# Kernel optimization log

Hardware: AMD Instinct MI355X
Metric: run time of the kernel (lower is better)

## Reference

```python
import jax, jax.numpy as jnp
import numpy as np

B, T, C = 4, 4096, 512
DFF = 4 * C


def setup_inputs() -> dict:
    key = jax.random.key(0)
    ks = jax.random.split(key, 8)
    s = 1.0 / np.sqrt(C)
    sf = 1.0 / np.sqrt(DFF)
    return {
        "inputs": jax.random.normal(ks[0], (B, T, C), dtype=jnp.float32),
        "Wq": jax.random.uniform(ks[1], (C, C), jnp.float32, -s, s),
        "Wk": jax.random.uniform(ks[2], (C, C), jnp.float32, -s, s),
        "Wv": jax.random.uniform(ks[3], (C, C), jnp.float32, -s, s),
        "W1": jax.random.uniform(ks[4], (C, DFF), jnp.float32, -s, s),
        "b1": jax.random.uniform(ks[5], (DFF,), jnp.float32, -s, s),
        "W2": jax.random.uniform(ks[6], (DFF, C), jnp.float32, -sf, sf),
        "b2": jax.random.uniform(ks[7], (C,), jnp.float32, -sf, sf),
    }


def reference(inputs, Wq, Wk, Wv, W1, b1, W2, b2):
    # Single-head causal self-attention, NO 1/sqrt(d) scaling (faithful to source)
    q = inputs @ Wq  # [B,T,C]
    k = inputs @ Wk
    v = inputs @ Wv
    scores = jnp.einsum("btc,bsc->bts", q, k)  # [B,T,T]
    Tdim = inputs.shape[1]
    causal = jnp.tril(jnp.ones((Tdim, Tdim), dtype=bool))
    scores = jnp.where(causal, scores, -jnp.inf)
    attn = jax.nn.softmax(scores, axis=-1)
    new_v = jnp.einsum("bts,bsc->btc", attn, v)  # [B,T,C]
    h = jax.nn.relu(new_v @ W1 + b1)  # [B,T,4C]
    return h @ W2 + b2  # [B,T,C]
```

## Files before the change

### kernel.cpp

```cpp
#include <hip/hip_runtime.h>
#include <stdint.h>

typedef __attribute__((ext_vector_type(8))) short bf16x8;
typedef __attribute__((ext_vector_type(8))) _Float16 f16x8;
typedef __attribute__((ext_vector_type(4))) float f32x4;
typedef __attribute__((ext_vector_type(4))) unsigned short us4;
typedef unsigned short u16;

#define DEVI static __device__ __forceinline__

#define Bb 4
#define Tt 4096
#define Cch 512
#define DFFd 2048
#define Mrows (Bb*Tt)
#define TRI 8650752ull

DEVI u16 f2bf(float f){
  union{float f;unsigned u;} v; v.f = f;
  unsigned r = v.u + 0x7FFFu + ((v.u >> 16) & 1u);
  return (u16)(r >> 16);
}
DEVI u16 f2h(float f){
  union{_Float16 h; u16 u;} v; v.h = (_Float16)f; return v.u;
}
DEVI float h2f(u16 h){
  union{u16 u; _Float16 h;} v; v.u = h; return (float)v.h;
}
DEVI size_t PANE(int q){ return (size_t)8192 * (size_t)(q*(q+1)); }

DEVI void gload16(const void* g, void* l){
  __builtin_amdgcn_global_load_lds((const __attribute__((address_space(1))) unsigned int*)g,
                                   (__attribute__((address_space(3))) unsigned int*)l, 16, 0, 0);
}

#define RDSWZ(l15, l4) (((l4)*16) ^ ((((l15) >> 1) & 3) << 4))

DEVI void stage128x64(const u16* __restrict__ base, int ld, char* lds, int w, int lane){
  #pragma unroll
  for(int i = 0; i < 4; i++){
    int s = i & 1;
    int chunk = w*2 + (i >> 1);
    int row = chunk*16 + (lane >> 2);
    int col = s*32 + (((lane & 3)*8) ^ (((lane >> 3) & 3) << 3));
    gload16(base + (size_t)row * ld + col, lds + s*8192 + chunk*1024 + lane*16);
  }
}
DEVI void stage64x64(const u16* __restrict__ base, int ld, char* lds, int w, int lane){
  #pragma unroll
  for(int i = 0; i < 2; i++){
    int s = i;
    int row = w*16 + (lane >> 2);
    int col = s*32 + (((lane & 3)*8) ^ (((lane >> 3) & 3) << 3));
    gload16(base + (size_t)row * ld + col, lds + s*4096 + w*1024 + lane*16);
  }
}

__global__ void k_cast_f16(const float* __restrict__ in, u16* __restrict__ out, int n){
  int i = (blockIdx.x * blockDim.x + threadIdx.x) * 4;
  if(i < n){
    float4 f = *(const float4*)(in + i);
    us4 o; o.x = f2h(f.x); o.y = f2h(f.y); o.z = f2h(f.z); o.w = f2h(f.w);
    *(us4*)(out + i) = o;
  }
}

__global__ void k_transpose_f32_f16(const float* __restrict__ in, u16* __restrict__ out,
                                    int inStride, int outStride){
  __shared__ float tile[32][33];
  int c0 = blockIdx.x * 32, r0 = blockIdx.y * 32;
  int tx = threadIdx.x, ty = threadIdx.y;
  #pragma unroll
  for(int j = 0; j < 4; j++)
    tile[ty + 8*j][tx] = in[(size_t)(r0 + ty + 8*j) * inStride + c0 + tx];
  __syncthreads();
  #pragma unroll
  for(int j = 0; j < 4; j++)
    out[(size_t)(c0 + ty + 8*j) * outStride + r0 + tx] = f2h(tile[tx][ty + 8*j]);
}

__global__ void k_transpose_f32_bf16(const float* __restrict__ in, u16* __restrict__ out,
                                     int inStride, int outStride){
  __shared__ float tile[32][33];
  int c0 = blockIdx.x * 32, r0 = blockIdx.y * 32;
  int tx = threadIdx.x, ty = threadIdx.y;
  #pragma unroll
  for(int j = 0; j < 4; j++)
    tile[ty + 8*j][tx] = in[(size_t)(r0 + ty + 8*j) * inStride + c0 + tx];
  __syncthreads();
  #pragma unroll
  for(int j = 0; j < 4; j++)
    out[(size_t)(c0 + ty + 8*j) * outStride + r0 + tx] = f2bf(tile[tx][ty + 8*j]);
}

DEVI void core_f16_64(const u16* __restrict__ A, const u16* __restrict__ B,
                      int lda, int ldb, int K, u16* As, u16* Bs, f32x4 (&acc)[4][4]){
  const int t = threadIdx.x;
  const int lane = t & 63, w = t >> 6;
  const int l15 = lane & 15, l4 = lane >> 4;
  const int wr = (w >> 1) * 64, wc = (w & 1) * 64;
  const int ro = RDSWZ(l15, l4);
  for(int kt = 0; kt < K; kt += 64){
    __syncthreads();
    stage128x64(A + kt, lda, (char*)As, w, lane);
    stage128x64(B + kt, ldb, (char*)Bs, w, lane);
    __syncthreads();
    f16x8 af[2][4], bfr[2][4];
    #pragma unroll
    for(int s = 0; s < 2; s++){
      #pragma unroll
      for(int mi = 0; mi < 4; mi++)
        af[s][mi] = *(const f16x8*)((const char*)As + s*8192 + (wr + mi*16 + l15)*64 + ro);
      #pragma unroll
      for(int ni = 0; ni < 4; ni++)
        bfr[s][ni] = *(const f16x8*)((const char*)Bs + s*8192 + (wc + ni*16 + l15)*64 + ro);
    }
    #pragma unroll
    for(int s = 0; s < 2; s++)
      #pragma unroll
      for(int mi = 0; mi < 4; mi++)
        #pragma unroll
        for(int ni = 0; ni < 4; ni++)
          acc[mi][ni] = __builtin_amdgcn_mfma_f32_16x16x32_f16(af[s][mi], bfr[s][ni], acc[mi][ni], 0, 0, 0);
  }
}

DEVI void core_bf16_64(const u16* __restrict__ A, const u16* __restrict__ B,
                       int lda, int ldb, int K, u16* As, u16* Bs, f32x4 (&acc)[4][4]){
  const int t = threadIdx.x;
  const int lane = t & 63, w = t >> 6;
  const int l15 = lane & 15, l4 = lane >> 4;
  const int wr = (w >> 1) * 64, wc = (w & 1) * 64;
  const int ro = RDSWZ(l15, l4);
  for(int kt = 0; kt < K; kt += 64){
    __syncthreads();
    stage128x64(A + kt, lda, (char*)As, w, lane);
    stage128x64(B + kt, ldb, (char*)Bs, w, lane);
    __syncthreads();
    bf16x8 af[2][4], bfr[2][4];
    #pragma unroll
    for(int s = 0; s < 2; s++){
      #pragma unroll
      for(int mi = 0; mi < 4; mi++)
        af[s][mi] = *(const bf16x8*)((const char*)As + s*8192 + (wr + mi*16 + l15)*64 + ro);
      #pragma unroll
      for(int ni = 0; ni < 4; ni++)
        bfr[s][ni] = *(const bf16x8*)((const char*)Bs + s*8192 + (wc + ni*16 + l15)*64 + ro);
    }
    #pragma unroll
    for(int s = 0; s < 2; s++)
      #pragma unroll
      for(int mi = 0; mi < 4; mi++)
        #pragma unroll
        for(int ni = 0; ni < 4; ni++)
          acc[mi][ni] = __builtin_amdgcn_mfma_f32_16x16x32_bf16(af[s][mi], bfr[s][ni], acc[mi][ni], 0, 0, 0);
  }
}

__global__ __launch_bounds__(256) void k_qkv(const u16* __restrict__ Xf,
                                             const u16* __restrict__ Wt,
                                             u16* __restrict__ QK,
                                             u16* __restrict__ Vg){
  __shared__ u16 As[8192], Bs[8192];
  const int bm = blockIdx.x * 128, bn = blockIdx.y * 128;
  f32x4 acc[4][4] = {};
  core_f16_64(Xf + (size_t)bm*512, Wt + (size_t)bn*512, 512, 512, 512, As, Bs, acc);
  const int t = threadIdx.x, lane = t & 63, w = t >> 6;
  const int l15 = lane & 15, l4 = lane >> 4;
  const int wr = (w >> 1) * 64, wc = (w & 1) * 64;
  #pragma unroll
  for(int mi = 0; mi < 4; mi++)
    #pragma unroll
    for(int ni = 0; ni < 4; ni++){
      int col = bn + wc + ni*16 + l15;
      #pragma unroll
      for(int r = 0; r < 4; r++){
        int row = bm + wr + mi*16 + l4*4 + r;
        u16 h = f2h(acc[mi][ni][r]);
        if(col < 1024){
          QK[(size_t)row * 1024 + col] = h;
        } else {
          int c = col - 1024;
          int b = row >> 12, tq = row & 4095;
          Vg[(size_t)b*Cch*Tt + ((size_t)(tq >> 5) * 512 + c) * 32 + (tq & 31)] = h;
        }
      }
    }
}

__global__ __launch_bounds__(256) void k_score(const u16* __restrict__ QK, int b0,
                                               u16* __restrict__ Sp){
  const int kt = blockIdx.x, qt = 31 - blockIdx.y;
  if(kt > qt) return;
  const int zb = blockIdx.z;
  const u16* QKb = QK + (size_t)(b0 + zb) * Tt * 1024;
  u16* Spz = Sp + (size_t)zb * TRI;
  __shared__ u16 As[8192], Bs[8192];
  const u16* A = QKb + (size_t)(qt*128) * 1024;
  const u16* B = QKb + (size_t)(kt*128) * 1024 + 512;
  f32x4 acc[4][4] = {};
  core_f16_64(A, B, 1024, 1024, 512, As, Bs, acc);
  const int t = threadIdx.x, lane = t & 63, w = t >> 6;
  const int l15 = lane & 15, l4 = lane >> 4;
  const int wr = (w >> 1) * 64, wc = (w & 1) * 64;
  const int ldc = (qt + 1) * 128;
  u16* C = Spz + PANE(qt) + (size_t)kt*128;
  const bool diag = (kt == qt);
  #pragma unroll
  for(int mi = 0; mi < 4; mi++)
    #pragma unroll
    for(int ni = 0; ni < 4; ni++){
      int cl = wc + ni*16 + l15;
      #pragma unroll
      for(int r = 0; r < 4; r++){
        int rl = wr + mi*16 + l4*4 + r;
        float v = acc[mi][ni][r];
        if(diag && cl > rl) v = -__builtin_inff();
        C[(size_t)rl * ldc + cl] = f2h(v);
      }
    }
}

__global__ __launch_bounds__(256) void k_softmax(u16* __restrict__ Sp){
  u16* Spz = Sp + (size_t)blockIdx.z * TRI;
  const int w = threadIdx.x >> 6, lane = threadIdx.x & 63;
  const int r = (1023 - blockIdx.x) * 4 + w;
  const int qt = r >> 7;
  const int nc = qt + 1;
  const int L = nc * 128;
  const size_t base = PANE(qt) + (size_t)(r & 127) * L;
  ushort2* rp = (ushort2*)(Spz + base);
  float2 v[32];
  float mx = -__builtin_inff();
  #pragma unroll
  for(int c = 0; c < 32; c++) if(c < nc){
    ushort2 h = rp[c*64 + lane];
    v[c].x = h2f(h.x); v[c].y = h2f(h.y);
    mx = fmaxf(mx, fmaxf(v[c].x, v[c].y));
  }
  #pragma unroll
  for(int s = 1; s < 64; s <<= 1) mx = fmaxf(mx, __shfl_xor(mx, s));
  float sm = 0.f;
  #pragma unroll
  for(int c = 0; c < 32; c++) if(c < nc){
    v[c].x = __expf(v[c].x - mx);
    v[c].y = __expf(v[c].y - mx);
    sm += v[c].x + v[c].y;
  }
  #pragma unroll
  for(int s = 1; s < 64; s <<= 1) sm += __shfl_xor(sm, s);
  const float inv = 1.f / sm;
  #pragma unroll
  for(int c = 0; c < 32; c++) if(c < nc){
    ushort2 o; o.x = f2h(v[c].x * inv); o.y = f2h(v[c].y * inv);
    rp[c*64 + lane] = o;
  }
}

__global__ __launch_bounds__(256) void k_pv(const u16* __restrict__ Pp, const u16* __restrict__ Vg,
                                            u16* __restrict__ NV, int b0){
  const int nc = blockIdx.x, qt = 31 - blockIdx.y, zb = blockIdx.z;
  const int L = (qt + 1) * 128;
  __shared__ u16 As[8192], Bs[8192];
  const u16* A = Pp + (size_t)zb * TRI + PANE(qt);
  const u16* Vgb = Vg + (size_t)(b0 + zb) * Cch * Tt;
  const int t = threadIdx.x, lane = t & 63, w = t >> 6;
  const int l15 = lane & 15, l4 = lane >> 4;
  const int wr = (w >> 1) * 64, wc = (w & 1) * 64;
  const int ro = RDSWZ(l15, l4);
  f32x4 acc[4][4] = {};
  for(int kt = 0; kt < L; kt += 64){
    __syncthreads();
    stage128x64(A + kt, L, (char*)As, w, lane);
    const size_t kvb0 = (size_t)(kt >> 5) * 16384 + nc*4096;
    #pragma unroll
    for(int i = 0; i < 4; i++){
      int s = i & 1;
      int p = w*2 + (i >> 1);
      int crow = p*16 + (lane >> 2);
      int kvo = ((lane & 3)*8) ^ (((lane >> 3) & 3) << 3);
      gload16(Vgb + kvb0 + (size_t)s*16384 + (size_t)crow*32 + kvo,
              (char*)Bs + s*8192 + p*1024 + lane*16);
    }
    __syncthreads();
    f16x8 af[2][4], bfr[2][4];
    #pragma unroll
    for(int s = 0; s < 2; s++){
      #pragma unroll
      for(int mi = 0; mi < 4; mi++)
        af[s][mi] = *(const f16x8*)((const char*)As + s*8192 + (wr + mi*16 + l15)*64 + ro);
      #pragma unroll
      for(int ni = 0; ni < 4; ni++)
        bfr[s][ni] = *(const f16x8*)((const char*)Bs + s*8192 + (wc + ni*16 + l15)*64 + ro);
    }
    #pragma unroll
    for(int s = 0; s < 2; s++)
      #pragma unroll
      for(int mi = 0; mi < 4; mi++)
        #pragma unroll
        for(int ni = 0; ni < 4; ni++)
          acc[mi][ni] = __builtin_amdgcn_mfma_f32_16x16x32_f16(af[s][mi], bfr[s][ni], acc[mi][ni], 0, 0, 0);
  }
  u16* Cb = NV + ((size_t)(b0 + zb) * Tt + qt*128) * Cch + nc*128;
  #pragma unroll
  for(int mi = 0; mi < 4; mi++)
    #pragma unroll
    for(int ni = 0; ni < 4; ni++){
      int cl = wc + ni*16 + l15;
      #pragma unroll
      for(int r = 0; r < 4; r++){
        int rl = wr + mi*16 + l4*4 + r;
        Cb[(size_t)rl * Cch + cl] = f2bf(acc[mi][ni][r]);
      }
    }
}

__global__ __launch_bounds__(256) void k_ffn1(const u16* __restrict__ A,
                                              const u16* __restrict__ Bt,
                                              u16* __restrict__ Hout,
                                              const float* __restrict__ bias){
  __shared__ u16 As[8192], Bs[8192];
  const int bm = blockIdx.x * 128, bn = blockIdx.y * 128;
  f32x4 acc[4][4] = {};
  core_bf16_64(A + (size_t)bm*512, Bt + (size_t)bn*512, 512, 512, 512, As, Bs, acc);
  const int t = threadIdx.x, lane = t & 63, w = t >> 6;
  const int l15 = lane & 15, l4 = lane >> 4;
  const int wr = (w >> 1) * 64, wc = (w & 1) * 64;
  #pragma unroll
  for(int mi = 0; mi < 4; mi++)
    #pragma unroll
    for(int ni = 0; ni < 4; ni++){
      int col = bn + wc + ni*16 + l15;
      float bv = bias[col];
      #pragma unroll
      for(int r = 0; r < 4; r++){
        int row = bm + wr + mi*16 + l4*4 + r;
        float v = acc[mi][ni][r] + bv;
        v = v > 0.f ? v : 0.f;
        Hout[(size_t)row * DFFd + col] = f2bf(v);
      }
    }
}

__global__ __launch_bounds__(256) void k_ffn2(const u16* __restrict__ A,
                                              const u16* __restrict__ Bt,
                                              float* __restrict__ out,
                                              const float* __restrict__ bias){
  __shared__ u16 As[8192], Bs[4096];
  const int bm = blockIdx.x * 128, bn = blockIdx.y * 64;
  const int t = threadIdx.x, lane = t & 63, w = t >> 6;
  const int l15 = lane & 15, l4 = lane >> 4;
  const int wr = (w >> 1) * 64, wc = (w & 1) * 32;
  const int ro = RDSWZ(l15, l4);
  const u16* Ap = A + (size_t)bm*2048;
  const u16* Bp = Bt + (size_t)bn*2048;
  f32x4 acc[4][2] = {};
  for(int kt = 0; kt < 2048; kt += 64){
    __syncthreads();
    stage128x64(Ap + kt, 2048, (char*)As, w, lane);
    stage64x64(Bp + kt, 2048, (char*)Bs, w, lane);
    __syncthreads();
    bf16x8 af[2][4], bfr[2][2];
    #pragma unroll
    for(int s = 0; s < 2; s++){
      #pragma unroll
      for(int mi = 0; mi < 4; mi++)
        af[s][mi] = *(const bf16x8*)((const char*)As + s*8192 + (wr + mi*16 + l15)*64 + ro);
      #pragma unroll
      for(int ni = 0; ni < 2; ni++)
        bfr[s][ni] = *(const bf16x8*)((const char*)Bs + s*4096 + (wc + ni*16 + l15)*64 + ro);
    }
    #pragma unroll
    for(int s = 0; s < 2; s++)
      #pragma unroll
      for(int mi = 0; mi < 4; mi++)
        #pragma unroll
        for(int ni = 0; ni < 2; ni++)
          acc[mi][ni] = __builtin_amdgcn_mfma_f32_16x16x32_bf16(af[s][mi], bfr[s][ni], acc[mi][ni], 0, 0, 0);
  }
  #pragma unroll
  for(int mi = 0; mi < 4; mi++)
    #pragma unroll
    for(int ni = 0; ni < 2; ni++){
      int col = bn + wc + ni*16 + l15;
      float bv = bias[col];
      #pragma unroll
      for(int r = 0; r < 4; r++){
        int row = bm + wr + mi*16 + l4*4 + r;
        out[(size_t)row * Cch + col] = acc[mi][ni][r] + bv;
      }
    }
}

extern "C" void kernel_launch(void* const* d_in, const int* in_sizes, int n_in,
                              void* d_out, int out_size, void* d_ws, size_t ws_size,
                              hipStream_t stream){
  (void)in_sizes; (void)n_in; (void)out_size;
  const float* X  = (const float*)d_in[0];
  const float* Wq = (const float*)d_in[1];
  const float* Wk = (const float*)d_in[2];
  const float* Wv = (const float*)d_in[3];
  const float* W1 = (const float*)d_in[4];
  const float* b1 = (const float*)d_in[5];
  const float* W2 = (const float*)d_in[6];
  const float* b2 = (const float*)d_in[7];
  float* out = (float*)d_out;

  const size_t MB = 1024ull*1024ull;
  const size_t PANE_B = (size_t)TRI * 2;
  char* ws = (char*)d_ws;

  int nb = 1;
  if(ws_size >= 4*PANE_B + 71*MB) nb = 4;
  else if(ws_size >= 2*PANE_B + 71*MB) nb = 2;

  u16*   Sp = (u16*)ws;
  u16*   Xf = (u16*)ws;
  u16*   H  = (u16*)ws;
  size_t off = (size_t)nb * PANE_B;
  u16*   QK   = (u16*)(ws + off);  off += 32*MB;
  u16*   Vg   = (u16*)(ws + off);  off += 16*MB;
  u16*   NV   = (u16*)(ws + off);  off += 16*MB;
  u16*   Wt   = (u16*)(ws + off);  off += 2*MB;
  u16*   W1t  = (u16*)(ws + off);  off += 2*MB;
  u16*   W2t  = (u16*)(ws + off);

  dim3 tb(32, 8);

  k_cast_f16<<<Mrows*Cch/4/256, 256, 0, stream>>>(X, Xf, Mrows*Cch);

  k_transpose_f32_f16<<<dim3(16,16), tb, 0, stream>>>(Wq, Wt,            512, 512);
  k_transpose_f32_f16<<<dim3(16,16), tb, 0, stream>>>(Wk, Wt +  512*512, 512, 512);
  k_transpose_f32_f16<<<dim3(16,16), tb, 0, stream>>>(Wv, Wt + 1024*512, 512, 512);
  k_transpose_f32_bf16<<<dim3(64,16), tb, 0, stream>>>(W1, W1t, 2048, 512);
  k_transpose_f32_bf16<<<dim3(16,64), tb, 0, stream>>>(W2, W2t, 512, 2048);

  k_qkv<<<dim3(128, 12), 256, 0, stream>>>(Xf, Wt, QK, Vg);

  for(int b0 = 0; b0 < Bb; b0 += nb){
    k_score<<<dim3(32, 32, nb), 256, 0, stream>>>(QK, b0, Sp);
    k_softmax<<<dim3(1024, 1, nb), 256, 0, stream>>>(Sp);
    k_pv<<<dim3(4, 32, nb), 256, 0, stream>>>(Sp, Vg, NV, b0);
  }

  k_ffn1<<<dim3(128, 16), 256, 0, stream>>>(NV, W1t, H, b1);
  k_ffn2<<<dim3(128, 8), 256, 0, stream>>>(H, W2t, out, b2);
}
```

Measured before the change: 342.0 us.

## Enlarge GEMM tiles to 256x128 with 8 waves for qkv, score, ffn1

Switches the qkv, score and ffn1 GEMM kernels from 128x128 tiles with 4 waves to 256x128 tiles with 8 waves. The B tile in LDS is shared across twice as many output rows, which halves B global traffic per output and the number of blocks. The score kernel adapts the causal triangle indexing so each half of the block writes its own 128-row pane and skips rows above the diagonal. The cost is more LDS per block, a larger block that may reduce occupancy, and idle waves on partially masked diagonal tiles.

```diff
diff --git a/kernel.cpp b/kernel.cpp
--- a/kernel.cpp
+++ b/kernel.cpp
@@ -35,6 +35,7 @@
 }
 
 #define RDSWZ(l15, l4) (((l4)*16) ^ ((((l15) >> 1) & 3) << 4))
+#define SRCSWZ(lane) ((((lane) & 3)*8) ^ ((((lane) >> 3) & 3) << 3))
 
 DEVI void stage128x64(const u16* __restrict__ base, int ld, char* lds, int w, int lane){
   #pragma unroll
@@ -42,7 +43,7 @@
     int s = i & 1;
     int chunk = w*2 + (i >> 1);
     int row = chunk*16 + (lane >> 2);
-    int col = s*32 + (((lane & 3)*8) ^ (((lane >> 3) & 3) << 3));
+    int col = s*32 + SRCSWZ(lane);
     gload16(base + (size_t)row * ld + col, lds + s*8192 + chunk*1024 + lane*16);
   }
 }
@@ -51,8 +52,28 @@
   for(int i = 0; i < 2; i++){
     int s = i;
     int row = w*16 + (lane >> 2);
-    int col = s*32 + (((lane & 3)*8) ^ (((lane >> 3) & 3) << 3));
+    int col = s*32 + SRCSWZ(lane);
     gload16(base + (size_t)row * ld + col, lds + s*4096 + w*1024 + lane*16);
+  }
+}
+
+DEVI void stage256x64_w8(const u16* __restrict__ base, int ld, char* lds, int w, int lane){
+  #pragma unroll
+  for(int i = 0; i < 4; i++){
+    int s = i & 1;
+    int chunk = w + (i >> 1)*8;
+    int row = chunk*16 + (lane >> 2);
+    int col = s*32 + SRCSWZ(lane);
+    gload16(base + (size_t)row * ld + col, lds + s*16384 + chunk*1024 + lane*16);
+  }
+}
+DEVI void stage128x64_w8(const u16* __restrict__ base, int ld, char* lds, int w, int lane){
+  #pragma unroll
+  for(int i = 0; i < 2; i++){
+    int s = i;
+    int row = w*16 + (lane >> 2);
+    int col = s*32 + SRCSWZ(lane);
+    gload16(base + (size_t)row * ld + col, lds + s*8192 + w*1024 + lane*16);
   }
 }
 
@@ -93,8 +114,8 @@
     out[(size_t)(c0 + ty + 8*j) * outStride + r0 + tx] = f2bf(tile[tx][ty + 8*j]);
 }
 
-DEVI void core_f16_64(const u16* __restrict__ A, const u16* __restrict__ B,
-                      int lda, int ldb, int K, u16* As, u16* Bs, f32x4 (&acc)[4][4]){
+DEVI void core_f16_256(const u16* __restrict__ A, const u16* __restrict__ B,
+                       int lda, int ldb, int K, u16* As, u16* Bs, f32x4 (&acc)[4][4]){
   const int t = threadIdx.x;
   const int lane = t & 63, w = t >> 6;
   const int l15 = lane & 15, l4 = lane >> 4;
@@ -102,15 +123,15 @@
   const int ro = RDSWZ(l15, l4);
   for(int kt = 0; kt < K; kt += 64){
     __syncthreads();
-    stage128x64(A + kt, lda, (char*)As, w, lane);
-    stage128x64(B + kt, ldb, (char*)Bs, w, lane);
+    stage256x64_w8(A + kt, lda, (char*)As, w, lane);
+    stage128x64_w8(B + kt, ldb, (char*)Bs, w, lane);
     __syncthreads();
     f16x8 af[2][4], bfr[2][4];
     #pragma unroll
     for(int s = 0; s < 2; s++){
       #pragma unroll
       for(int mi = 0; mi < 4; mi++)
-        af[s][mi] = *(const f16x8*)((const char*)As + s*8192 + (wr + mi*16 + l15)*64 + ro);
+        af[s][mi] = *(const f16x8*)((const char*)As + s*16384 + (wr + mi*16 + l15)*64 + ro);
       #pragma unroll
       for(int ni = 0; ni < 4; ni++)
         bfr[s][ni] = *(const f16x8*)((const char*)Bs + s*8192 + (wc + ni*16 + l15)*64 + ro);
@@ -125,8 +146,8 @@
   }
 }
 
-DEVI void core_bf16_64(const u16* __restrict__ A, const u16* __restrict__ B,
-                       int lda, int ldb, int K, u16* As, u16* Bs, f32x4 (&acc)[4][4]){
+DEVI void core_bf16_256(const u16* __restrict__ A, const u16* __restrict__ B,
+                        int lda, int ldb, int K, u16* As, u16* Bs, f32x4 (&acc)[4][4]){
   const int t = threadIdx.x;
   const int lane = t & 63, w = t >> 6;
   const int l15 = lane & 15, l4 = lane >> 4;
@@ -134,15 +155,15 @@
   const int ro = RDSWZ(l15, l4);
   for(int kt = 0; kt < K; kt += 64){
     __syncthreads();
-    stage128x64(A + kt, lda, (char*)As, w, lane);
-    stage128x64(B + kt, ldb, (char*)Bs, w, lane);
+    stage256x64_w8(A + kt, lda, (char*)As, w, lane);
+    stage128x64_w8(B + kt, ldb, (char*)Bs, w, lane);
     __syncthreads();
     bf16x8 af[2][4], bfr[2][4];
     #pragma unroll
     for(int s = 0; s < 2; s++){
       #pragma unroll
       for(int mi = 0; mi < 4; mi++)
-        af[s][mi] = *(const bf16x8*)((const char*)As + s*8192 + (wr + mi*16 + l15)*64 + ro);
+        af[s][mi] = *(const bf16x8*)((const char*)As + s*16384 + (wr + mi*16 + l15)*64 + ro);
       #pragma unroll
       for(int ni = 0; ni < 4; ni++)
         bfr[s][ni] = *(const bf16x8*)((const char*)Bs + s*8192 + (wc + ni*16 + l15)*64 + ro);
@@ -157,14 +178,14 @@
   }
 }
 
-__global__ __launch_bounds__(256) void k_qkv(const u16* __restrict__ Xf,
+__global__ __launch_bounds__(512) void k_qkv(const u16* __restrict__ Xf,
                                              const u16* __restrict__ Wt,
                                              u16* __restrict__ QK,
                                              u16* __restrict__ Vg){
-  __shared__ u16 As[8192], Bs[8192];
-  const int bm = blockIdx.x * 128, bn = blockIdx.y * 128;
+  __shared__ u16 As[16384], Bs[8192];
+  const int bm = blockIdx.x * 256, bn = blockIdx.y * 128;
   f32x4 acc[4][4] = {};
-  core_f16_64(Xf + (size_t)bm*512, Wt + (size_t)bn*512, 512, 512, 512, As, Bs, acc);
+  core_f16_256(Xf + (size_t)bm*512, Wt + (size_t)bn*512, 512, 512, 512, As, Bs, acc);
   const int t = threadIdx.x, lane = t & 63, w = t >> 6;
   const int l15 = lane & 15, l4 = lane >> 4;
   const int wr = (w >> 1) * 64, wc = (w & 1) * 64;
@@ -188,24 +209,27 @@
     }
 }
 
-__global__ __launch_bounds__(256) void k_score(const u16* __restrict__ QK, int b0,
+__global__ __launch_bounds__(512) void k_score(const u16* __restrict__ QK, int b0,
                                                u16* __restrict__ Sp){
-  const int kt = blockIdx.x, qt = 31 - blockIdx.y;
-  if(kt > qt) return;
+  const int kt = blockIdx.x, qy = 15 - blockIdx.y;
+  if(kt > 2*qy + 1) return;
   const int zb = blockIdx.z;
   const u16* QKb = QK + (size_t)(b0 + zb) * Tt * 1024;
   u16* Spz = Sp + (size_t)zb * TRI;
-  __shared__ u16 As[8192], Bs[8192];
-  const u16* A = QKb + (size_t)(qt*128) * 1024;
+  __shared__ u16 As[16384], Bs[8192];
+  const u16* A = QKb + (size_t)(qy*256) * 1024;
   const u16* B = QKb + (size_t)(kt*128) * 1024 + 512;
   f32x4 acc[4][4] = {};
-  core_f16_64(A, B, 1024, 1024, 512, As, Bs, acc);
+  core_f16_256(A, B, 1024, 1024, 512, As, Bs, acc);
   const int t = threadIdx.x, lane = t & 63, w = t >> 6;
   const int l15 = lane & 15, l4 = lane >> 4;
   const int wr = (w >> 1) * 64, wc = (w & 1) * 64;
-  const int ldc = (qt + 1) * 128;
-  u16* C = Spz + PANE(qt) + (size_t)kt*128;
-  const bool diag = (kt == qt);
+  const int qt_row = qy*2 + (wr >> 7);
+  if(kt > qt_row) return;
+  const int ldc = (qt_row + 1) * 128;
+  const int rof = wr & 64;
+  u16* C = Spz + PANE(qt_row) + (size_t)kt*128;
+  const bool diag = (kt == qt_row);
   #pragma unroll
   for(int mi = 0; mi < 4; mi++)
     #pragma unroll
@@ -213,7 +237,7 @@
       int cl = wc + ni*16 + l15;
       #pragma unroll
       for(int r = 0; r < 4; r++){
-        int rl = wr + mi*16 + l4*4 + r;
+        int rl = rof + mi*16 + l4*4 + r;
         float v = acc[mi][ni][r];
         if(diag && cl > rl) v = -__builtin_inff();
         C[(size_t)rl * ldc + cl] = f2h(v);
@@ -278,7 +302,7 @@
       int s = i & 1;
       int p = w*2 + (i >> 1);
       int crow = p*16 + (lane >> 2);
-      int kvo = ((lane & 3)*8) ^ (((lane >> 3) & 3) << 3);
+      int kvo = SRCSWZ(lane);
       gload16(Vgb + kvb0 + (size_t)s*16384 + (size_t)crow*32 + kvo,
               (char*)Bs + s*8192 + p*1024 + lane*16);
     }
@@ -315,14 +339,14 @@
     }
 }
 
-__global__ __launch_bounds__(256) void k_ffn1(const u16* __restrict__ A,
+__global__ __launch_bounds__(512) void k_ffn1(const u16* __restrict__ A,
                                               const u16* __restrict__ Bt,
                                               u16* __restrict__ Hout,
                                               const float* __restrict__ bias){
-  __shared__ u16 As[8192], Bs[8192];
-  const int bm = blockIdx.x * 128, bn = blockIdx.y * 128;
+  __shared__ u16 As[16384], Bs[8192];
+  const int bm = blockIdx.x * 256, bn = blockIdx.y * 128;
   f32x4 acc[4][4] = {};
-  core_bf16_64(A + (size_t)bm*512, Bt + (size_t)bn*512, 512, 512, 512, As, Bs, acc);
+  core_bf16_256(A + (size_t)bm*512, Bt + (size_t)bn*512, 512, 512, 512, As, Bs, acc);
   const int t = threadIdx.x, lane = t & 63, w = t >> 6;
   const int l15 = lane & 15, l4 = lane >> 4;
   const int wr = (w >> 1) * 64, wc = (w & 1) * 64;
@@ -435,14 +459,14 @@
   k_transpose_f32_bf16<<<dim3(64,16), tb, 0, stream>>>(W1, W1t, 2048, 512);
   k_transpose_f32_bf16<<<dim3(16,64), tb, 0, stream>>>(W2, W2t, 512, 2048);
 
-  k_qkv<<<dim3(128, 12), 256, 0, stream>>>(Xf, Wt, QK, Vg);
+  k_qkv<<<dim3(64, 12), 512, 0, stream>>>(Xf, Wt, QK, Vg);
 
   for(int b0 = 0; b0 < Bb; b0 += nb){
-    k_score<<<dim3(32, 32, nb), 256, 0, stream>>>(QK, b0, Sp);
+    k_score<<<dim3(32, 16, nb), 512, 0, stream>>>(QK, b0, Sp);
     k_softmax<<<dim3(1024, 1, nb), 256, 0, stream>>>(Sp);
     k_pv<<<dim3(4, 32, nb), 256, 0, stream>>>(Sp, Vg, NV, b0);
   }
 
-  k_ffn1<<<dim3(128, 16), 256, 0, stream>>>(NV, W1t, H, b1);
+  k_ffn1<<<dim3(64, 16), 512, 0, stream>>>(NV, W1t, H, b1);
   k_ffn2<<<dim3(128, 8), 256, 0, stream>>>(H, W2t, out, b2);
 }
```

Result: no change. 341.8 us (-0.0%).
